# Kernel tuning notes

Measured on AMD Instinct MI355X. Metric: run time of the kernel, lower is better.

The kernel has to match this reference:

```python
import jax, jax.numpy as jnp
import numpy as np
import math

INPUT_SIZE = 256
HIDDEN_SIZE = 1024
TIMESTEPS = 32768


def setup_inputs() -> dict:
    key = jax.random.key(0)
    ks = jax.random.split(key, 7)
    stdv = 1.0 / math.sqrt(HIDDEN_SIZE)
    u = lambda k, shape: jax.random.uniform(k, shape, jnp.float32, -stdv, stdv)
    return {
        "input_data": jax.random.normal(ks[0], (TIMESTEPS, 1, INPUT_SIZE), jnp.float32),
        "weight_ih": u(ks[1], (HIDDEN_SIZE, INPUT_SIZE)),
        "weight_hh": u(ks[2], (HIDDEN_SIZE, HIDDEN_SIZE)),
        "weight": u(ks[3], (HIDDEN_SIZE,)),
        "bias_ih": u(ks[4], (HIDDEN_SIZE,)),
        "bias_hh": u(ks[5], (HIDDEN_SIZE,)),
        "bias": u(ks[6], (HIDDEN_SIZE,)),
    }


def reference(input_data, weight_ih, weight_hh, weight, bias_ih, bias_hh, bias):
    # input_data: [T, 1, F] (batch must be 1, as in the original flatten-based matmuls)
    T, B, F = input_data.shape
    x = input_data.reshape(T, F)
    # Precompute all input projections as one GEMM: [T, H]
    xW = x @ weight_ih.T

    def step(h, xw):
        hW = weight_hh @ h  # [H]
        h_new = jnp.tanh(weight * xw * hW + bias_ih * xw + bias_hh * hW + bias)
        return h_new, h_new

    h0 = jnp.zeros((weight_hh.shape[0],), dtype=input_data.dtype)
    _, ys = jax.lax.scan(step, h0, xW)
    return ys[:, None, :]  # [T, 1, H]
```

## Files before the change

### kernel.cpp

```cpp
#include <hip/hip_runtime.h>
#include <hip/hip_bf16.h>
#include <stdint.h>

#define T_STEPS 32768
#define HID 1024
#define FIN 256
#define NB_SCAN 32
#define NB_HEAT 28
#define RPB 32
#define RPW 8
#define WORDS (HID / 2)

typedef unsigned long long ull;

__global__ __launch_bounds__(256) void gemm_xw(const float* __restrict__ x,
                                               const float* __restrict__ wih,
                                               float* __restrict__ out) {
    __shared__ float As[32][132];
    __shared__ float Bs[32][132];
    const int tid = threadIdx.x;
    const int m0 = blockIdx.y * 128;
    const int n0 = blockIdx.x * 128;
    const int tm = tid >> 4, tn = tid & 15;
    const int lr = tid >> 1, lc = (tid & 1) * 16;

    float acc[8][8];
#pragma unroll
    for (int i = 0; i < 8; ++i)
#pragma unroll
        for (int j = 0; j < 8; ++j) acc[i][j] = 0.f;

    for (int kk = 0; kk < FIN; kk += 32) {
#pragma unroll
        for (int u = 0; u < 4; ++u) {
            float4 av = *reinterpret_cast<const float4*>(
                &x[(size_t)(m0 + lr) * FIN + kk + lc + 4 * u]);
            float4 bv = *reinterpret_cast<const float4*>(
                &wih[(size_t)(n0 + lr) * FIN + kk + lc + 4 * u]);
            As[lc + 4 * u + 0][lr] = av.x;
            As[lc + 4 * u + 1][lr] = av.y;
            As[lc + 4 * u + 2][lr] = av.z;
            As[lc + 4 * u + 3][lr] = av.w;
            Bs[lc + 4 * u + 0][lr] = bv.x;
            Bs[lc + 4 * u + 1][lr] = bv.y;
            Bs[lc + 4 * u + 2][lr] = bv.z;
            Bs[lc + 4 * u + 3][lr] = bv.w;
        }
        __syncthreads();
#pragma unroll
        for (int k = 0; k < 32; ++k) {
            const float4* Ak = reinterpret_cast<const float4*>(&As[k][0]);
            const float4* Bk = reinterpret_cast<const float4*>(&Bs[k][0]);
            float4 a0 = Ak[tm * 2], a1 = Ak[tm * 2 + 1];
            float4 b0 = Bk[tn * 2], b1 = Bk[tn * 2 + 1];
            float a[8] = {a0.x, a0.y, a0.z, a0.w, a1.x, a1.y, a1.z, a1.w};
            float b[8] = {b0.x, b0.y, b0.z, b0.w, b1.x, b1.y, b1.z, b1.w};
#pragma unroll
            for (int i = 0; i < 8; ++i)
#pragma unroll
                for (int j = 0; j < 8; ++j) acc[i][j] = fmaf(a[i], b[j], acc[i][j]);
        }
        __syncthreads();
    }
#pragma unroll
    for (int i = 0; i < 8; ++i) {
        float4 o0 = make_float4(acc[i][0], acc[i][1], acc[i][2], acc[i][3]);
        float4 o1 = make_float4(acc[i][4], acc[i][5], acc[i][6], acc[i][7]);
        float* op = &out[(size_t)(m0 + tm * 8 + i) * HID + n0 + tn * 8];
        *reinterpret_cast<float4*>(op) = o0;
        *reinterpret_cast<float4*>(op + 4) = o1;
    }
}

__device__ __forceinline__ float fast_tanh(float x) {
    float cx = fminf(fmaxf(x, -16.f), 16.f);
    float e = __builtin_amdgcn_exp2f(cx * 2.8853900817779268f);
    return (e - 1.f) * __builtin_amdgcn_rcpf(e + 1.f);
}

__device__ __forceinline__ void poll8(const ull* __restrict__ src, int lane,
                                      ull (&v)[8]) {
#pragma unroll
    for (int i = 0; i < 8; ++i)
        v[i] = __hip_atomic_load(src + lane + 64 * i, __ATOMIC_RELAXED,
                                 __HIP_MEMORY_SCOPE_AGENT);
}

__device__ __forceinline__ bool check8(const ull (&v)[8], unsigned expb) {
    unsigned d = 0;
#pragma unroll
    for (int i = 0; i < 8; ++i) d |= (((unsigned)v[i]) ^ expb) & 0xFFu;
    return d == 0;
}

__device__ void heater_body(const int* quit, int tid) {
    float a0 = tid * 0.001f + 1.f, a1 = a0 + 1.f, a2 = a0 + 2.f, a3 = a0 + 3.f;
    float a4 = a0 + 4.f, a5 = a0 + 5.f, a6 = a0 + 6.f, a7 = a0 + 7.f;
    for (int it = 0; it < 300000; ++it) {
#pragma unroll 64
        for (int u = 0; u < 64; ++u) {
            a0 = fmaf(a0, 1.0000001f, 0.5f);
            a1 = fmaf(a1, 1.0000001f, 0.5f);
            a2 = fmaf(a2, 1.0000001f, 0.5f);
            a3 = fmaf(a3, 1.0000001f, 0.5f);
            a4 = fmaf(a4, 1.0000001f, 0.5f);
            a5 = fmaf(a5, 1.0000001f, 0.5f);
            a6 = fmaf(a6, 1.0000001f, 0.5f);
            a7 = fmaf(a7, 1.0000001f, 0.5f);
        }
        if (__hip_atomic_load(quit, __ATOMIC_RELAXED, __HIP_MEMORY_SCOPE_AGENT))
            break;
    }
    asm volatile("" ::"v"(a0), "v"(a1), "v"(a2), "v"(a3), "v"(a4), "v"(a5),
                 "v"(a6), "v"(a7));
}

__global__ __launch_bounds__(256, 1) void scan_rnn(
    const float* __restrict__ whh, const float* __restrict__ wgt,
    const float* __restrict__ bih, const float* __restrict__ bhh,
    const float* __restrict__ bb, float* __restrict__ out,
    ull* __restrict__ hbuf, int* __restrict__ quit) {
    if (blockIdx.x >= NB_SCAN) {
        heater_body(quit, threadIdx.x);
        return;
    }
    __shared__ ull hshw[WORDS];
    const int lane = threadIdx.x & 63;
    const int wv = threadIdx.x >> 6;
    const int r0 = blockIdx.x * RPB + wv * RPW;
    const int rr = r0 + (lane & 7);

    float wreg[RPW][16];
#pragma unroll
    for (int j = 0; j < RPW; ++j)
#pragma unroll
        for (int i = 0; i < 16; ++i)
            wreg[j][i] = whh[(size_t)(r0 + j) * HID + lane + 64 * i];

    const float cw = wgt[rr], cbi = bih[rr], cbh = bhh[rr], cb = bb[rr];
    float xw_cur = out[rr];

    for (int t = 0; t < T_STEPS; ++t) {
        if (wv == 0) {
            const ull* src = hbuf + (size_t)(t & 1) * WORDS;
            const unsigned expb = (unsigned)t & 0xFFu;
            ull va[8], vb[8];
            poll8(src, lane, va);
            for (;;) {
                poll8(src, lane, vb);
                if (check8(va, expb)) {
#pragma unroll
                    for (int i = 0; i < 8; ++i) hshw[lane + 64 * i] = va[i];
                    break;
                }
                poll8(src, lane, va);
                if (check8(vb, expb)) {
#pragma unroll
                    for (int i = 0; i < 8; ++i) hshw[lane + 64 * i] = vb[i];
                    break;
                }
                __builtin_amdgcn_s_sleep(1);
            }
        }
        __syncthreads();

        const float* hf = (const float*)(&hshw[0]);
        float hval[16];
#pragma unroll
        for (int i = 0; i < 16; ++i) hval[i] = hf[lane + 64 * i];

        float acc[RPW];
#pragma unroll
        for (int j = 0; j < RPW; ++j) acc[j] = 0.f;
#pragma unroll
        for (int i = 0; i < 16; ++i)
#pragma unroll
            for (int j = 0; j < RPW; ++j)
                acc[j] = fmaf(wreg[j][i], hval[i], acc[j]);

#pragma unroll
        for (int m = 1; m < 8; m <<= 1)
#pragma unroll
            for (int j = 0; j < RPW; ++j) acc[j] += __shfl_xor(acc[j], m, 64);
        float y = acc[0];
#pragma unroll
        for (int j = 1; j < RPW; ++j) y = ((lane & 7) == j) ? acc[j] : y;
#pragma unroll
        for (int m = 8; m < 64; m <<= 1) y += __shfl_xor(y, m, 64);

        const float arg = fmaf(fmaf(cw, xw_cur, cbh), y, fmaf(cbi, xw_cur, cb));
        const float hn = fast_tanh(arg);
        const float hnp = __shfl_xor(hn, 1, 64);

        if (lane < 8) {
            if ((lane & 1) == 0) {
                unsigned lo = (__float_as_uint(hn) & 0xFFFFFF00u) |
                              ((unsigned)(t + 1) & 0xFFu);
                ull pv = ((ull)__float_as_uint(hnp) << 32) | (ull)lo;
                __hip_atomic_store(
                    hbuf + (size_t)((t + 1) & 1) * WORDS + (r0 >> 1) +
                        (lane >> 1),
                    pv, __ATOMIC_RELAXED, __HIP_MEMORY_SCOPE_AGENT);
            }
            out[(size_t)t * HID + rr] = hn;
        }
        const int nt = t < T_STEPS - 1 ? t + 1 : t;
        xw_cur = out[(size_t)nt * HID + rr];
    }
    if (blockIdx.x == 0 && threadIdx.x == 0)
        __hip_atomic_store(quit, 1, __ATOMIC_RELAXED, __HIP_MEMORY_SCOPE_AGENT);
}

extern "C" void kernel_launch(void* const* d_in, const int* in_sizes, int n_in,
                              void* d_out, int out_size, void* d_ws, size_t ws_size,
                              hipStream_t stream) {
    const float* x = (const float*)d_in[0];
    const float* wih = (const float*)d_in[1];
    const float* whh = (const float*)d_in[2];
    const float* wgt = (const float*)d_in[3];
    const float* bih = (const float*)d_in[4];
    const float* bhh = (const float*)d_in[5];
    const float* bb = (const float*)d_in[6];
    float* out = (float*)d_out;

    ull* hbuf = (ull*)d_ws;
    int* quit = (int*)((char*)d_ws + 2 * WORDS * sizeof(ull));
    hipMemsetAsync(d_ws, 0, 2 * WORDS * sizeof(ull) + 128, stream);

    dim3 ggrid(HID / 128, T_STEPS / 128);
    gemm_xw<<<ggrid, 256, 0, stream>>>(x, wih, out);

    scan_rnn<<<NB_SCAN + NB_HEAT, 256, 0, stream>>>(whh, wgt, bih, bhh, bb,
                                                    out, hbuf, quit);
}
```

Baseline: 65.32 ms.

## Replicate hidden-state broadcast buffer per consumer block to avoid shared polling

Each scan block now polls its own private copy of the double-buffered hidden-state array, and every producer wavefront writes its packed, tagged values into all 32 consumer copies (each of 64 lanes issues two stores). This spreads polling traffic across separate cache lines instead of having all blocks hammer the same lines, which is meant to cut contention and latency in the per-timestep cross-block synchronization. The cost is 32x more store traffic per step and a larger workspace to memset.

Measured after the change: 64.70 ms. No clear change (-0.9%).

```diff
diff --git a/kernel.cpp b/kernel.cpp
--- a/kernel.cpp
+++ b/kernel.cpp
@@ -142,7 +142,8 @@
 
     for (int t = 0; t < T_STEPS; ++t) {
         if (wv == 0) {
-            const ull* src = hbuf + (size_t)(t & 1) * WORDS;
+            const ull* src =
+                hbuf + ((size_t)(t & 1) * NB_SCAN + blockIdx.x) * WORDS;
             const unsigned expb = (unsigned)t & 0xFFu;
             ull va[8], vb[8];
             poll8(src, lane, va);
@@ -190,20 +191,24 @@
 
         const float arg = fmaf(fmaf(cw, xw_cur, cbh), y, fmaf(cbi, xw_cur, cb));
         const float hn = fast_tanh(arg);
-        const float hnp = __shfl_xor(hn, 1, 64);
-
-        if (lane < 8) {
-            if ((lane & 1) == 0) {
-                unsigned lo = (__float_as_uint(hn) & 0xFFFFFF00u) |
-                              ((unsigned)(t + 1) & 0xFFu);
-                ull pv = ((ull)__float_as_uint(hnp) << 32) | (ull)lo;
-                __hip_atomic_store(
-                    hbuf + (size_t)((t + 1) & 1) * WORDS + (r0 >> 1) +
-                        (lane >> 1),
-                    pv, __ATOMIC_RELAXED, __HIP_MEMORY_SCOPE_AGENT);
-            }
-            out[(size_t)t * HID + rr] = hn;
-        }
+
+        {
+            const int j = lane & 3;
+            const float lo_f = __shfl(hn, 2 * j, 8);
+            const float hi_f = __shfl(hn, 2 * j + 1, 8);
+            const unsigned tagb = (unsigned)(t + 1) & 0xFFu;
+            const unsigned lo = (__float_as_uint(lo_f) & 0xFFFFFF00u) | tagb;
+            const ull pv = ((ull)__float_as_uint(hi_f) << 32) | (ull)lo;
+            const int widx = (r0 >> 1) + j;
+            ull* dstbase =
+                hbuf + (size_t)((t + 1) & 1) * NB_SCAN * WORDS + widx;
+            const int cons = lane >> 2;
+            __hip_atomic_store(dstbase + (size_t)cons * WORDS, pv,
+                               __ATOMIC_RELAXED, __HIP_MEMORY_SCOPE_AGENT);
+            __hip_atomic_store(dstbase + (size_t)(cons + 16) * WORDS, pv,
+                               __ATOMIC_RELAXED, __HIP_MEMORY_SCOPE_AGENT);
+        }
+        if (lane < 8) out[(size_t)t * HID + rr] = hn;
         const int nt = t < T_STEPS - 1 ? t + 1 : t;
         xw_cur = out[(size_t)nt * HID + rr];
     }
@@ -224,8 +229,9 @@
     float* out = (float*)d_out;
 
     ull* hbuf = (ull*)d_ws;
-    int* quit = (int*)((char*)d_ws + 2 * WORDS * sizeof(ull));
-    hipMemsetAsync(d_ws, 0, 2 * WORDS * sizeof(ull) + 128, stream);
+    const size_t hbytes = (size_t)2 * NB_SCAN * WORDS * sizeof(ull);
+    int* quit = (int*)((char*)d_ws + hbytes);
+    hipMemsetAsync(d_ws, 0, hbytes + 128, stream);
 
     dim3 ggrid(HID / 128, T_STEPS / 128);
     gemm_xw<<<ggrid, 256, 0, stream>>>(x, wih, out);
```
